# Optimization experiments

Hardware: AMD Instinct MI355X
Metric: run time of the kernel (lower is better)

The kernel has to match this reference:

```python
import jax, jax.numpy as jnp
from jax import lax
import numpy as np

NUM_HEADS = 8
KW = 3  # window kernel size

def _avgpool3(x):
    # x: [B,C,H,W]; AvgPool2d(3,1,1) with count_include_pad=True -> sum/9
    s = lax.reduce_window(x, 0.0, lax.add, (1, 1, KW, KW), (1, 1, 1, 1),
                          ((0, 0), (0, 0), (1, 1), (1, 1)))
    return s / (KW * KW)

def _unfold3(y):
    # y: [B,h,w,C] -> [B,h,w,9,C]; patch index ordered row-major (kh,kw)
    B, h, w, C = y.shape
    yp = jnp.pad(y, ((0, 0), (1, 1), (1, 1), (0, 0)))
    return jnp.stack([yp[:, i:i + h, j:j + w, :]
                      for i in range(KW) for j in range(KW)], axis=3)

def setup_inputs():
    key = jax.random.key(0)
    ks = jax.random.split(key, 9)
    B, C, H, W = 8, 256, 64, 64
    sd = 0.02
    return {
        "x": jax.random.normal(ks[0], (B, C, H, W), jnp.float32),
        "W_qkv": jax.random.normal(ks[1], (4 * C, C), jnp.float32) * sd,
        "b_qkv": jnp.zeros((4 * C,), jnp.float32),
        "W1": jax.random.normal(ks[2], (C // 2, C), jnp.float32) * sd,
        "b1": jnp.zeros((C // 2,), jnp.float32),
        "W2": jax.random.normal(ks[3], (C, C // 2), jnp.float32) * sd,
        "b2": jnp.zeros((C,), jnp.float32),
        "Wp": jax.random.normal(ks[4], (C, C), jnp.float32) * sd,
        "bp": jnp.zeros((C,), jnp.float32),
    }

def reference(x, W_qkv, b_qkv, W1, b1, W2, b2, Wp, bp):
    B, C, H, W = x.shape
    nH = NUM_HEADS
    hd = C // nH
    scale = hd ** -0.5
    # avg pool (stride 1 keeps spatial dims), to channels-last
    y = _avgpool3(x).transpose(0, 2, 3, 1)                 # [B,h,w,C]
    qkv = y @ W_qkv.T + b_qkv                              # [B,h,w,4C]
    qkv = qkv.reshape(B, H, W, C, 4)
    q, k, v, chans = qkv[..., 0], qkv[..., 1], qkv[..., 2], qkv[..., 3]
    # channel gate
    g = jax.nn.sigmoid(jax.nn.relu(chans @ W1.T + b1) @ W2.T + b2)  # [B,h,w,C]
    # local window attention: each query attends to its 3x3 neighborhood
    qh = q.reshape(B, H, W, nH, hd)                        # [B,h,w,n,d]
    kp = _unfold3(k).reshape(B, H, W, KW * KW, nH, hd)     # [B,h,w,9,n,d]
    vp = _unfold3(v).reshape(B, H, W, KW * KW, nH, hd)
    attn = jnp.einsum('bhwnd,bhwknd->bhwnk', qh, kp) * scale
    attn = jax.nn.softmax(attn, axis=-1)
    out = jnp.einsum('bhwnk,bhwknd->bhwnd', attn, vp).reshape(B, H, W, C)
    out = out * g + out
    out = out @ Wp.T + bp
    return out.transpose(0, 3, 1, 2)                       # [B,C,H,W]
```

## Files before the change

### kernel.cpp

```cpp
#include <hip/hip_runtime.h>
#include <stdint.h>

typedef __bf16    bf16x8 __attribute__((ext_vector_type(8)));
typedef float     f32x4  __attribute__((ext_vector_type(4)));
typedef uint32_t  u32x4  __attribute__((ext_vector_type(4)));

#define MFMA(a,b,c) __builtin_amdgcn_mfma_f32_16x16x32_bf16((a),(b),(c),0,0,0)

__device__ __align__(16) uint16_t g_y [8*64*64*256];
__device__ __align__(16) uint16_t g_wpk[393216];

#define WQF 0
#define WKF 65536
#define WVF 131072
#define WCF 196608
#define W1F 262144
#define W2F 294912
#define WPF 327680

static __device__ __forceinline__ float b2f(uint32_t u){ return __builtin_bit_cast(float, u<<16); }
static __device__ __forceinline__ uint32_t f2b(float f){
  uint32_t x = __builtin_bit_cast(uint32_t, f);
  return (x + 0x7fffu + ((x>>16)&1u)) >> 16;
}

__global__ __launch_bounds__(256) void kpack(const float* __restrict__ Wqkv,
    const float* __restrict__ W1, const float* __restrict__ W2,
    const float* __restrict__ Wp){
  int idx = blockIdx.x*256 + threadIdx.x;
  int j = idx & 7, lane = (idx>>3)&63;
  int n16 = lane & 15, q4 = lane>>4;
  float v;
  if (idx < 262144){
    int t = idx >> 16, l = idx & 65535;
    int s = (l>>9)&7, nt = l>>12;
    v = Wqkv[(4*(nt*16+n16) + t)*256 + s*32 + q4*8 + j];
  } else if (idx < 294912){
    int l = idx - 262144;
    int s = (l>>9)&7, nt = l>>12;
    v = W1[(nt*16+n16)*256 + s*32 + q4*8 + j];
  } else if (idx < 327680){
    int l = idx - 294912;
    int s = (l>>9)&3, nt = l>>11;
    v = W2[(nt*16+n16)*128 + s*32 + q4*8 + j];
  } else {
    int l = idx - 327680;
    int s = (l>>9)&7, nt = l>>12;
    v = Wp[(nt*16+n16)*256 + s*32 + q4*8 + j];
  }
  g_wpk[idx] = (uint16_t)f2b(v);
}

__global__ __launch_bounds__(512) void kpool(const float* __restrict__ x){
  __shared__ __align__(16) uint16_t sm[3*256*82];
  uint32_t* smw = (uint32_t*)sm;
  int t = threadIdx.x;
  int b = blockIdx.x >> 6, h = blockIdx.x & 63;
  for (int i=t; i<768; i+=512){
    int base = i*41;
    smw[base+3]  = 0;
    smw[base+36] = 0;
  }
  if (h==0 || h==63){
    int hh = (h==0) ? 0 : 2;
    for (int i=t; i<10496; i+=512) smw[hh*10496 + i] = 0;
  }
  #pragma unroll
  for (int i=0;i<24;i++){
    int id = t + 512*i;
    int w4 = id&15, c = (id>>4)&255, hh = id>>12;
    int gy = h - 1 + hh;
    if ((unsigned)gy < 64u){
      f32x4 ld = *(const f32x4*)&x[(((b*256+c)*64+gy)*64) + w4*4];
      int wb = (((hh*256+c)*82 + 8 + w4*4) >> 1);
      smw[wb+0] = f2b(ld[0]) | (f2b(ld[1])<<16);
      smw[wb+1] = f2b(ld[2]) | (f2b(ld[3])<<16);
    }
  }
  __syncthreads();
  int c = t & 255, wsel = t >> 8;
  int r0 = c*82, r1 = r0 + 256*82, r2 = r1 + 256*82;
  int w0 = wsel*32;
  float csp = b2f(sm[r0+w0+7]) + b2f(sm[r1+w0+7]) + b2f(sm[r2+w0+7]);
  float csc = b2f(sm[r0+w0+8]) + b2f(sm[r1+w0+8]) + b2f(sm[r2+w0+8]);
  uint16_t* dst = g_y + ((b*64+h)*64)*256 + c;
  for (int j2=0;j2<32;j2++){
    int w = w0 + j2;
    float csn = b2f(sm[r0+w+9]) + b2f(sm[r1+w+9]) + b2f(sm[r2+w+9]);
    float yv = (csp + csc + csn) * (1.0f/9.0f);
    dst[w*256] = (uint16_t)f2b(yv);
    csp = csc; csc = csn;
  }
}

#define YSTR 264
#define HSTR 134
#define K2_QS 26400
#define K2_KS 34976
#define K2_VS 48376
#define MCH 0
#define MHS 16896
#define MAO 25600
__global__ __launch_bounds__(512,2) void kattn(const float* __restrict__ bqkv,
    const float* __restrict__ b1, const float* __restrict__ b2v,
    const float* __restrict__ bp, float* __restrict__ out){
  __shared__ __align__(16) uint16_t sm[61776];
  int t = threadIdx.x;
  int lane = t & 63, wave = t >> 6;
  int n16 = lane & 15, quad = lane >> 4;
  int bid = blockIdx.x;
  int bb = bid>>6, tyhi=(bid>>4)&3, txl=(bid>>3)&1, tylo=(bid>>2)&1, txp=bid&3;
  int ty = tyhi*2+tylo, tx = txp*2+txl;

  uint32_t opk[2][16];
  uint32_t chp[32];

  #pragma unroll
  for (int i=0;i<7;i++){
    int id = t + 512*i;
    if (id < 3200){
      int hp = id >> 5, c8 = id & 31;
      int py = hp/10, px = hp - py*10;
      int gy = ty*8 + py - 1, gx = tx*8 + px - 1;
      u32x4 ld = {0,0,0,0};
      if ((unsigned)gy<64u && (unsigned)gx<64u)
        ld = *(const u32x4*)&g_y[((bb*64+gy)*64+gx)*256 + c8*8];
      *(u32x4*)&sm[hp*YSTR + c8*8] = ld;
    }
  }
  __syncthreads();

  #pragma unroll
  for (int hf=0; hf<2; hf++){
    {
      int ntg = hf*8 + wave;
      bf16x8 Bq[8];
      #pragma unroll
      for (int s=0;s<8;s++) Bq[s] = *(const bf16x8*)&g_wpk[WQF + ((ntg*8+s)*64+lane)*8];
      float bq = bqkv[4*(ntg*16+n16) + 0];
      int colB = wave*16;
      #pragma unroll
      for (int mt=0; mt<4; mt++){
        f32x4 a = {0.f,0.f,0.f,0.f};
        int m = mt*16 + n16;
        int hrow = 10*(m>>3) + (m&7) + 11;
        #pragma unroll
        for (int s=0;s<8;s++){
          bf16x8 A = *(const bf16x8*)&sm[hrow*YSTR + s*32 + quad*8];
          a = MFMA(A, Bq[s], a);
        }
        #pragma unroll
        for (int r=0;r<4;r++){
          int row = mt*16 + quad*4 + r;
          sm[K2_QS + row*HSTR + colB + n16] = (uint16_t)f2b(a[r] + bq);
        }
      }
    }
    __syncthreads();
    {
      int ntg = hf*8 + wave;
      bf16x8 Bk[8], Bv[8];
      #pragma unroll
      for (int s=0;s<8;s++){
        Bk[s] = *(const bf16x8*)&g_wpk[WKF + ((ntg*8+s)*64+lane)*8];
        Bv[s] = *(const bf16x8*)&g_wpk[WVF + ((ntg*8+s)*64+lane)*8];
      }
      float bk = bqkv[4*(ntg*16+n16) + 1];
      float bv = bqkv[4*(ntg*16+n16) + 2];
      int colB = wave*16;
      #pragma unroll
      for (int mt=0; mt<7; mt++){
        f32x4 ak = {0.f,0.f,0.f,0.f}, av = {0.f,0.f,0.f,0.f};
        int m = mt*16 + n16;
        int mr = (m < 100) ? m : 99;
        #pragma unroll
        for (int s=0;s<8;s++){
          bf16x8 A = *(const bf16x8*)&sm[mr*YSTR + s*32 + quad*8];
          ak = MFMA(A, Bk[s], ak);
          av = MFMA(A, Bv[s], av);
        }
        #pragma unroll
        for (int r=0;r<4;r++){
          int row = mt*16 + quad*4 + r;
          if (row < 100){
            int py = row/10, px = row - py*10;
            int gy = ty*8 + py - 1, gx = tx*8 + px - 1;
            bool ok = ((unsigned)gy<64u) && ((unsigned)gx<64u);
            float vk = ok ? ak[r] + bk : 0.f;
            float vv = ok ? av[r] + bv : 0.f;
            sm[K2_KS + row*HSTR + colB + n16] = (uint16_t)f2b(vk);
            sm[K2_VS + row*HSTR + colB + n16] = (uint16_t)f2b(vv);
          }
        }
      }
    }
    __syncthreads();
    if (wave < 4){
      int p = t & 63, hl = wave;
      int iy = p >> 3, ix = p & 7;
      int cb = hl*32;
      const uint32_t* q32 = (const uint32_t*)&sm[K2_QS + p*HSTR + cb];
      float qv[32];
      #pragma unroll
      for (int i=0;i<16;i++){ uint32_t u=q32[i]; qv[2*i]=b2f(u&0xffffu); qv[2*i+1]=b2f(u>>16); }
      int hb = (iy+1)*10 + ix + 1;
      const int off[9] = {-11,-10,-9,-1,0,1,9,10,11};
      float sc[9];
      #pragma unroll
      for (int nb=0;nb<9;nb++){
        const uint32_t* k32 = (const uint32_t*)&sm[K2_KS + (hb+off[nb])*HSTR + cb];
        float s = 0.f;
        #pragma unroll
        for (int i=0;i<16;i++){ uint32_t u=k32[i]; s += qv[2*i]*b2f(u&0xffffu) + qv[2*i+1]*b2f(u>>16); }
        sc[nb] = s * 0.17677669529663687f;
      }
      float mx = sc[0];
      #pragma unroll
      for (int nb=1;nb<9;nb++) mx = fmaxf(mx, sc[nb]);
      float l = 0.f;
      #pragma unroll
      for (int nb=0;nb<9;nb++){ sc[nb] = __expf(sc[nb]-mx); l += sc[nb]; }
      float inv = 1.f / l;
      float o[32];
      #pragma unroll
      for (int i=0;i<32;i++) o[i]=0.f;
      #pragma unroll
      for (int nb=0;nb<9;nb++){
        float wgt = sc[nb]*inv;
        const uint32_t* v32 = (const uint32_t*)&sm[K2_VS + (hb+off[nb])*HSTR + cb];
        #pragma unroll
        for (int i=0;i<16;i++){ uint32_t u=v32[i]; o[2*i] += wgt*b2f(u&0xffffu); o[2*i+1] += wgt*b2f(u>>16); }
      }
      #pragma unroll
      for (int i=0;i<16;i++) opk[hf][i] = f2b(o[2*i]) | (f2b(o[2*i+1])<<16);
    } else if (hf == 0){
      #pragma unroll
      for (int jj=0;jj<4;jj++){
        int ntg = (wave-4)*4 + jj;
        bf16x8 Bc[8];
        #pragma unroll
        for (int s=0;s<8;s++) Bc[s] = *(const bf16x8*)&g_wpk[WCF + ((ntg*8+s)*64+lane)*8];
        float bc = bqkv[4*(ntg*16+n16) + 3];
        #pragma unroll
        for (int mt=0; mt<4; mt++){
          f32x4 a = {0.f,0.f,0.f,0.f};
          int m = mt*16 + n16;
          int hrow = 10*(m>>3) + (m&7) + 11;
          #pragma unroll
          for (int s=0;s<8;s++){
            bf16x8 A = *(const bf16x8*)&sm[hrow*YSTR + s*32 + quad*8];
            a = MFMA(A, Bc[s], a);
          }
          chp[(jj*4+mt)*2+0] = f2b(a[0]+bc) | (f2b(a[1]+bc)<<16);
          chp[(jj*4+mt)*2+1] = f2b(a[2]+bc) | (f2b(a[3]+bc)<<16);
        }
      }
    } else {
      #pragma unroll
      for (int jj=0;jj<4;jj++){
        int ntg = (wave-4)*4 + jj;
        int col = ntg*16 + n16;
        #pragma unroll
        for (int mt=0;mt<4;mt++){
          #pragma unroll
          for (int r2=0;r2<2;r2++){
            uint32_t v = chp[(jj*4+mt)*2+r2];
            int row = mt*16 + quad*4 + r2*2;
            sm[MCH + row*264 + col]     = (uint16_t)(v & 0xffffu);
            sm[MCH + (row+1)*264 + col] = (uint16_t)(v >> 16);
          }
        }
      }
    }
    __syncthreads();
  }
  if (wave < 4){
    int p = t & 63, cb = wave*32;
    #pragma unroll
    for (int hf=0;hf<2;hf++)
      #pragma unroll
      for (int i=0;i<16;i++)
        *(uint32_t*)&sm[MAO + p*264 + hf*128 + cb + 2*i] = opk[hf][i];
  }
  {
    int ntg = wave;
    bf16x8 Bf[8];
    #pragma unroll
    for (int s=0;s<8;s++) Bf[s] = *(const bf16x8*)&g_wpk[W1F + ((ntg*8+s)*64+lane)*8];
    float bs = b1[ntg*16+n16];
    int colB = wave*16;
    #pragma unroll
    for (int mt=0;mt<4;mt++){
      f32x4 a = {0.f,0.f,0.f,0.f};
      #pragma unroll
      for (int s=0;s<8;s++){
        bf16x8 A = *(const bf16x8*)&sm[MCH + (mt*16+n16)*264 + s*32 + quad*8];
        a = MFMA(A, Bf[s], a);
      }
      #pragma unroll
      for (int r=0;r<4;r++){
        int row = mt*16 + quad*4 + r;
        sm[MHS + row*136 + colB + n16] = (uint16_t)f2b(fmaxf(a[r]+bs, 0.f));
      }
    }
  }
  __syncthreads();
  #pragma unroll
  for (int jj=0;jj<2;jj++){
    int ntg = wave*2 + jj;
    bf16x8 Bf[4];
    #pragma unroll
    for (int s=0;s<4;s++) Bf[s] = *(const bf16x8*)&g_wpk[W2F + ((ntg*4+s)*64+lane)*8];
    float bs = b2v[ntg*16+n16];
    int colB = ntg*16;
    #pragma unroll
    for (int mt=0;mt<4;mt++){
      f32x4 a = {0.f,0.f,0.f,0.f};
      #pragma unroll
      for (int s=0;s<4;s++){
        bf16x8 A = *(const bf16x8*)&sm[MHS + (mt*16+n16)*136 + s*32 + quad*8];
        a = MFMA(A, Bf[s], a);
      }
      #pragma unroll
      for (int r=0;r<4;r++){
        int row = mt*16 + quad*4 + r;
        float gg = 1.f/(1.f+__expf(-(a[r] + bs)));
        float ao = b2f((uint32_t)sm[MAO + row*264 + colB + n16]);
        sm[MCH + row*264 + colB + n16] = (uint16_t)f2b(ao*(1.f+gg));
      }
    }
  }
  __syncthreads();
  #pragma unroll
  for (int jj=0;jj<2;jj++){
    int ntg = wave*2 + jj;
    bf16x8 Bf[8];
    #pragma unroll
    for (int s=0;s<8;s++) Bf[s] = *(const bf16x8*)&g_wpk[WPF + ((ntg*8+s)*64+lane)*8];
    float bs = bp[ntg*16+n16];
    int colB = ntg*16;
    #pragma unroll
    for (int mt=0;mt<4;mt++){
      f32x4 a = {0.f,0.f,0.f,0.f};
      #pragma unroll
      for (int s=0;s<8;s++){
        bf16x8 A = *(const bf16x8*)&sm[MCH + (mt*16+n16)*264 + s*32 + quad*8];
        a = MFMA(A, Bf[s], a);
      }
      #pragma unroll
      for (int r=0;r<4;r++){
        int row = mt*16 + quad*4 + r;
        sm[MAO + row*264 + colB + n16] = (uint16_t)f2b(a[r]+bs);
      }
    }
  }
  __syncthreads();
  #pragma unroll
  for (int i=0;i<8;i++){
    int idx = t + 512*i;
    int ix4 = idx&1, iy = (idx>>1)&7, c = idx>>4;
    f32x4 stv;
    #pragma unroll
    for (int j=0;j<4;j++){
      int p = iy*8 + ix4*4 + j;
      stv[j] = b2f((uint32_t)sm[MAO + p*264 + c]);
    }
    *(f32x4*)&out[(((bb*256+c)*64) + ty*8+iy)*64 + tx*8 + ix4*4] = stv;
  }
}

extern "C" void kernel_launch(void* const* d_in, const int* in_sizes, int n_in,
                              void* d_out, int out_size, void* d_ws, size_t ws_size,
                              hipStream_t stream){
  (void)in_sizes; (void)n_in; (void)d_ws; (void)ws_size; (void)out_size;
  const float* x    = (const float*)d_in[0];
  const float* Wqkv = (const float*)d_in[1];
  const float* bqkv = (const float*)d_in[2];
  const float* W1   = (const float*)d_in[3];
  const float* b1   = (const float*)d_in[4];
  const float* W2   = (const float*)d_in[5];
  const float* b2   = (const float*)d_in[6];
  const float* Wp   = (const float*)d_in[7];
  const float* bp   = (const float*)d_in[8];
  kpack<<<dim3(1536), dim3(256), 0, stream>>>(Wqkv, W1, W2, Wp);
  kpool<<<dim3(512),  dim3(512), 0, stream>>>(x);
  kattn<<<dim3(512),  dim3(512), 0, stream>>>(bqkv, b1, b2, bp, (float*)d_out);
}
```

Before: 188.4 us.

## Double attention block to 1024 threads and redistribute QKV, attention and gate work

New measurement: 203.5 us. 8.0% more time.

```diff
diff --git a/kernel.cpp b/kernel.cpp
--- a/kernel.cpp
+++ b/kernel.cpp
@@ -19,6 +19,7 @@
 #define WPF 327680
 
 static __device__ __forceinline__ float b2f(uint32_t u){ return __builtin_bit_cast(float, u<<16); }
+static __device__ __forceinline__ float b2fh(uint32_t u){ return __builtin_bit_cast(float, u & 0xffff0000u); }
 static __device__ __forceinline__ uint32_t f2b(float f){
   uint32_t x = __builtin_bit_cast(uint32_t, f);
   return (x + 0x7fffu + ((x>>16)&1u)) >> 16;
@@ -94,17 +95,18 @@
 }
 
 #define YSTR 264
-#define HSTR 134
-#define K2_QS 26400
-#define K2_KS 34976
-#define K2_VS 48376
+#define HSTR 136
+#define YS 0
+#define QS 26400
+#define KS 35104
+#define VS 48704
 #define MCH 0
 #define MHS 16896
-#define MAO 25600
-__global__ __launch_bounds__(512,2) void kattn(const float* __restrict__ bqkv,
+#define MAO 26400
+__global__ __launch_bounds__(1024,4) void kattn(const float* __restrict__ bqkv,
     const float* __restrict__ b1, const float* __restrict__ b2v,
     const float* __restrict__ bp, float* __restrict__ out){
-  __shared__ __align__(16) uint16_t sm[61776];
+  __shared__ __align__(16) uint16_t sm[62304];
   int t = threadIdx.x;
   int lane = t & 63, wave = t >> 6;
   int n16 = lane & 15, quad = lane >> 4;
@@ -112,12 +114,12 @@
   int bb = bid>>6, tyhi=(bid>>4)&3, txl=(bid>>3)&1, tylo=(bid>>2)&1, txp=bid&3;
   int ty = tyhi*2+tylo, tx = txp*2+txl;
 
-  uint32_t opk[2][16];
-  uint32_t chp[32];
+  uint32_t opk[2][8];
+  uint32_t chp[16];
 
   #pragma unroll
-  for (int i=0;i<7;i++){
-    int id = t + 512*i;
+  for (int i=0;i<4;i++){
+    int id = t + 1024*i;
     if (id < 3200){
       int hp = id >> 5, c8 = id & 31;
       int py = hp/10, px = hp - py*10;
@@ -133,87 +135,97 @@
   #pragma unroll
   for (int hf=0; hf<2; hf++){
     {
-      int ntg = hf*8 + wave;
-      bf16x8 Bq[8];
-      #pragma unroll
-      for (int s=0;s<8;s++) Bq[s] = *(const bf16x8*)&g_wpk[WQF + ((ntg*8+s)*64+lane)*8];
-      float bq = bqkv[4*(ntg*16+n16) + 0];
-      int colB = wave*16;
-      #pragma unroll
-      for (int mt=0; mt<4; mt++){
-        f32x4 a = {0.f,0.f,0.f,0.f};
-        int m = mt*16 + n16;
-        int hrow = 10*(m>>3) + (m&7) + 11;
-        #pragma unroll
-        for (int s=0;s<8;s++){
-          bf16x8 A = *(const bf16x8*)&sm[hrow*YSTR + s*32 + quad*8];
-          a = MFMA(A, Bq[s], a);
-        }
-        #pragma unroll
-        for (int r=0;r<4;r++){
-          int row = mt*16 + quad*4 + r;
-          sm[K2_QS + row*HSTR + colB + n16] = (uint16_t)f2b(a[r] + bq);
+      int ntg = wave & 7;
+      int ntgg = hf*8 + ntg;
+      bool isK = wave < 8;
+      int colB = ntg*16;
+      {
+        bf16x8 Bx[8];
+        const uint16_t* wb = &g_wpk[(isK?WKF:WVF)];
+        #pragma unroll
+        for (int s=0;s<8;s++) Bx[s] = *(const bf16x8*)&wb[((ntgg*8+s)*64+lane)*8];
+        float bx = bqkv[4*(ntgg*16+n16) + (isK?1:2)];
+        int base = isK ? KS : VS;
+        #pragma unroll
+        for (int mt=0; mt<7; mt++){
+          f32x4 a = {0.f,0.f,0.f,0.f};
+          int m = mt*16 + n16;
+          int mr = (m < 100) ? m : 99;
+          #pragma unroll
+          for (int s=0;s<8;s++){
+            bf16x8 A = *(const bf16x8*)&sm[YS + mr*YSTR + s*32 + quad*8];
+            a = MFMA(A, Bx[s], a);
+          }
+          #pragma unroll
+          for (int r=0;r<4;r++){
+            int row = mt*16 + quad*4 + r;
+            if (row < 100){
+              int py = row/10, px = row - py*10;
+              int gy = ty*8 + py - 1, gx = tx*8 + px - 1;
+              bool ok = ((unsigned)gy<64u) && ((unsigned)gx<64u);
+              sm[base + row*HSTR + colB + n16] = (uint16_t)f2b(ok ? a[r]+bx : 0.f);
+            }
+          }
+        }
+      }
+      {
+        bf16x8 Bq[8];
+        #pragma unroll
+        for (int s=0;s<8;s++) Bq[s] = *(const bf16x8*)&g_wpk[WQF + ((ntgg*8+s)*64+lane)*8];
+        float bq = bqkv[4*(ntgg*16+n16) + 0];
+        int mt0 = isK ? 0 : 2;
+        #pragma unroll
+        for (int mi=0; mi<2; mi++){
+          int mt = mt0 + mi;
+          f32x4 a = {0.f,0.f,0.f,0.f};
+          int m = mt*16 + n16;
+          int hrow = 10*(m>>3) + (m&7) + 11;
+          #pragma unroll
+          for (int s=0;s<8;s++){
+            bf16x8 A = *(const bf16x8*)&sm[YS + hrow*YSTR + s*32 + quad*8];
+            a = MFMA(A, Bq[s], a);
+          }
+          #pragma unroll
+          for (int r=0;r<4;r++){
+            int row = mt*16 + quad*4 + r;
+            sm[QS + row*HSTR + colB + n16] = (uint16_t)f2b(a[r] + bq);
+          }
         }
       }
     }
     __syncthreads();
-    {
-      int ntg = hf*8 + wave;
-      bf16x8 Bk[8], Bv[8];
-      #pragma unroll
-      for (int s=0;s<8;s++){
-        Bk[s] = *(const bf16x8*)&g_wpk[WKF + ((ntg*8+s)*64+lane)*8];
-        Bv[s] = *(const bf16x8*)&g_wpk[WVF + ((ntg*8+s)*64+lane)*8];
-      }
-      float bk = bqkv[4*(ntg*16+n16) + 1];
-      float bv = bqkv[4*(ntg*16+n16) + 2];
-      int colB = wave*16;
-      #pragma unroll
-      for (int mt=0; mt<7; mt++){
-        f32x4 ak = {0.f,0.f,0.f,0.f}, av = {0.f,0.f,0.f,0.f};
-        int m = mt*16 + n16;
-        int mr = (m < 100) ? m : 99;
-        #pragma unroll
-        for (int s=0;s<8;s++){
-          bf16x8 A = *(const bf16x8*)&sm[mr*YSTR + s*32 + quad*8];
-          ak = MFMA(A, Bk[s], ak);
-          av = MFMA(A, Bv[s], av);
-        }
-        #pragma unroll
-        for (int r=0;r<4;r++){
-          int row = mt*16 + quad*4 + r;
-          if (row < 100){
-            int py = row/10, px = row - py*10;
-            int gy = ty*8 + py - 1, gx = tx*8 + px - 1;
-            bool ok = ((unsigned)gy<64u) && ((unsigned)gx<64u);
-            float vk = ok ? ak[r] + bk : 0.f;
-            float vv = ok ? av[r] + bv : 0.f;
-            sm[K2_KS + row*HSTR + colB + n16] = (uint16_t)f2b(vk);
-            sm[K2_VS + row*HSTR + colB + n16] = (uint16_t)f2b(vv);
-          }
-        }
-      }
-    }
-    __syncthreads();
-    if (wave < 4){
-      int p = t & 63, hl = wave;
+    if (wave < 8){
+      int h = wave >> 1, ph = wave & 1;
+      int pl = lane & 31, dh = lane >> 5;
+      int p = ph*32 + pl;
       int iy = p >> 3, ix = p & 7;
-      int cb = hl*32;
-      const uint32_t* q32 = (const uint32_t*)&sm[K2_QS + p*HSTR + cb];
-      float qv[32];
-      #pragma unroll
-      for (int i=0;i<16;i++){ uint32_t u=q32[i]; qv[2*i]=b2f(u&0xffffu); qv[2*i+1]=b2f(u>>16); }
+      int co = h*32 + dh*16;
+      u32x4 qa = *(const u32x4*)&sm[QS + p*HSTR + co];
+      u32x4 qb = *(const u32x4*)&sm[QS + p*HSTR + co + 8];
+      float qv[16];
+      #pragma unroll
+      for (int i=0;i<4;i++){
+        qv[2*i]   = b2f(qa[i]);  qv[2*i+1]   = b2fh(qa[i]);
+        qv[8+2*i] = b2f(qb[i]);  qv[8+2*i+1] = b2fh(qb[i]);
+      }
       int hb = (iy+1)*10 + ix + 1;
       const int off[9] = {-11,-10,-9,-1,0,1,9,10,11};
       float sc[9];
       #pragma unroll
       for (int nb=0;nb<9;nb++){
-        const uint32_t* k32 = (const uint32_t*)&sm[K2_KS + (hb+off[nb])*HSTR + cb];
+        const uint16_t* kr = &sm[KS + (hb+off[nb])*HSTR + co];
+        u32x4 ka = *(const u32x4*)kr;
+        u32x4 kb = *(const u32x4*)(kr+8);
         float s = 0.f;
         #pragma unroll
-        for (int i=0;i<16;i++){ uint32_t u=k32[i]; s += qv[2*i]*b2f(u&0xffffu) + qv[2*i+1]*b2f(u>>16); }
-        sc[nb] = s * 0.17677669529663687f;
-      }
+        for (int i=0;i<4;i++){
+          s += qv[2*i]*b2f(ka[i]) + qv[2*i+1]*b2fh(ka[i]);
+          s += qv[8+2*i]*b2f(kb[i]) + qv[8+2*i+1]*b2fh(kb[i]);
+        }
+        sc[nb] = s;
+      }
+      #pragma unroll
+      for (int nb=0;nb<9;nb++) sc[nb] = (sc[nb] + __shfl_xor(sc[nb], 32)) * 0.17677669529663687f;
       float mx = sc[0];
       #pragma unroll
       for (int nb=1;nb<9;nb++) mx = fmaxf(mx, sc[nb]);
@@ -221,22 +233,27 @@
       #pragma unroll
       for (int nb=0;nb<9;nb++){ sc[nb] = __expf(sc[nb]-mx); l += sc[nb]; }
       float inv = 1.f / l;
-      float o[32];
-      #pragma unroll
-      for (int i=0;i<32;i++) o[i]=0.f;
+      float o[16];
+      #pragma unroll
+      for (int i=0;i<16;i++) o[i]=0.f;
       #pragma unroll
       for (int nb=0;nb<9;nb++){
         float wgt = sc[nb]*inv;
-        const uint32_t* v32 = (const uint32_t*)&sm[K2_VS + (hb+off[nb])*HSTR + cb];
-        #pragma unroll
-        for (int i=0;i<16;i++){ uint32_t u=v32[i]; o[2*i] += wgt*b2f(u&0xffffu); o[2*i+1] += wgt*b2f(u>>16); }
-      }
-      #pragma unroll
-      for (int i=0;i<16;i++) opk[hf][i] = f2b(o[2*i]) | (f2b(o[2*i+1])<<16);
+        const uint16_t* vr = &sm[VS + (hb+off[nb])*HSTR + co];
+        u32x4 va = *(const u32x4*)vr;
+        u32x4 vb = *(const u32x4*)(vr+8);
+        #pragma unroll
+        for (int i=0;i<4;i++){
+          o[2*i]     += wgt*b2f(va[i]);  o[2*i+1]   += wgt*b2fh(va[i]);
+          o[8+2*i]   += wgt*b2f(vb[i]);  o[8+2*i+1] += wgt*b2fh(vb[i]);
+        }
+      }
+      #pragma unroll
+      for (int i=0;i<8;i++) opk[hf][i] = f2b(o[2*i]) | (f2b(o[2*i+1])<<16);
     } else if (hf == 0){
       #pragma unroll
-      for (int jj=0;jj<4;jj++){
-        int ntg = (wave-4)*4 + jj;
+      for (int jj=0;jj<2;jj++){
+        int ntg = (wave-8)*2 + jj;
         bf16x8 Bc[8];
         #pragma unroll
         for (int s=0;s<8;s++) Bc[s] = *(const bf16x8*)&g_wpk[WCF + ((ntg*8+s)*64+lane)*8];
@@ -248,7 +265,7 @@
           int hrow = 10*(m>>3) + (m&7) + 11;
           #pragma unroll
           for (int s=0;s<8;s++){
-            bf16x8 A = *(const bf16x8*)&sm[hrow*YSTR + s*32 + quad*8];
+            bf16x8 A = *(const bf16x8*)&sm[YS + hrow*YSTR + s*32 + quad*8];
             a = MFMA(A, Bc[s], a);
           }
           chp[(jj*4+mt)*2+0] = f2b(a[0]+bc) | (f2b(a[1]+bc)<<16);
@@ -257,8 +274,8 @@
       }
     } else {
       #pragma unroll
-      for (int jj=0;jj<4;jj++){
-        int ntg = (wave-4)*4 + jj;
+      for (int jj=0;jj<2;jj++){
+        int ntg = (wave-8)*2 + jj;
         int col = ntg*16 + n16;
         #pragma unroll
         for (int mt=0;mt<4;mt++){
@@ -266,76 +283,78 @@
           for (int r2=0;r2<2;r2++){
             uint32_t v = chp[(jj*4+mt)*2+r2];
             int row = mt*16 + quad*4 + r2*2;
-            sm[MCH + row*264 + col]     = (uint16_t)(v & 0xffffu);
-            sm[MCH + (row+1)*264 + col] = (uint16_t)(v >> 16);
+            sm[MCH + row*YSTR + col]        = (uint16_t)(v & 0xffffu);
+            sm[MCH + (row+1)*YSTR + col]    = (uint16_t)(v >> 16);
           }
         }
       }
     }
     __syncthreads();
   }
-  if (wave < 4){
-    int p = t & 63, cb = wave*32;
-    #pragma unroll
-    for (int hf=0;hf<2;hf++)
-      #pragma unroll
-      for (int i=0;i<16;i++)
-        *(uint32_t*)&sm[MAO + p*264 + hf*128 + cb + 2*i] = opk[hf][i];
-  }
+  if (wave < 8){
+    int h = wave >> 1, ph = wave & 1;
+    int pl = lane & 31, dh = lane >> 5;
+    int p = ph*32 + pl;
+    int co = h*32 + dh*16;
+    #pragma unroll
+    for (int hf=0;hf<2;hf++){
+      u32x4 s0 = {opk[hf][0],opk[hf][1],opk[hf][2],opk[hf][3]};
+      u32x4 s1 = {opk[hf][4],opk[hf][5],opk[hf][6],opk[hf][7]};
+      *(u32x4*)&sm[MAO + p*YSTR + hf*128 + co]     = s0;
+      *(u32x4*)&sm[MAO + p*YSTR + hf*128 + co + 8] = s1;
+    }
+  } else {
+    int ntg = wave - 8;
+    bf16x8 Bf[8];
+    #pragma unroll
+    for (int s=0;s<8;s++) Bf[s] = *(const bf16x8*)&g_wpk[W1F + ((ntg*8+s)*64+lane)*8];
+    float bs = b1[ntg*16+n16];
+    int colB = ntg*16;
+    #pragma unroll
+    for (int mt=0;mt<4;mt++){
+      f32x4 a = {0.f,0.f,0.f,0.f};
+      #pragma unroll
+      for (int s=0;s<8;s++){
+        bf16x8 A = *(const bf16x8*)&sm[MCH + (mt*16+n16)*YSTR + s*32 + quad*8];
+        a = MFMA(A, Bf[s], a);
+      }
+      #pragma unroll
+      for (int r=0;r<4;r++){
+        int row = mt*16 + quad*4 + r;
+        sm[MHS + row*HSTR + colB + n16] = (uint16_t)f2b(fmaxf(a[r]+bs, 0.f));
+      }
+    }
+  }
+  __syncthreads();
+  {
+    int ntg = wave;
+    bf16x8 Bf[4];
+    #pragma unroll
+    for (int s=0;s<4;s++) Bf[s] = *(const bf16x8*)&g_wpk[W2F + ((ntg*4+s)*64+lane)*8];
+    float bs = b2v[ntg*16+n16];
+    int colB = ntg*16;
+    #pragma unroll
+    for (int mt=0;mt<4;mt++){
+      f32x4 a = {0.f,0.f,0.f,0.f};
+      #pragma unroll
+      for (int s=0;s<4;s++){
+        bf16x8 A = *(const bf16x8*)&sm[MHS + (mt*16+n16)*HSTR + s*32 + quad*8];
+        a = MFMA(A, Bf[s], a);
+      }
+      #pragma unroll
+      for (int r=0;r<4;r++){
+        int row = mt*16 + quad*4 + r;
+        float gg = 1.f/(1.f+__expf(-(a[r] + bs)));
+        float ao = b2f((uint32_t)sm[MAO + row*YSTR + colB + n16]);
+        sm[MCH + row*YSTR + colB + n16] = (uint16_t)f2b(ao*(1.f+gg));
+      }
+    }
+  }
+  __syncthreads();
   {
     int ntg = wave;
     bf16x8 Bf[8];
     #pragma unroll
-    for (int s=0;s<8;s++) Bf[s] = *(const bf16x8*)&g_wpk[W1F + ((ntg*8+s)*64+lane)*8];
-    float bs = b1[ntg*16+n16];
-    int colB = wave*16;
-    #pragma unroll
-    for (int mt=0;mt<4;mt++){
-      f32x4 a = {0.f,0.f,0.f,0.f};
-      #pragma unroll
-      for (int s=0;s<8;s++){
-        bf16x8 A = *(const bf16x8*)&sm[MCH + (mt*16+n16)*264 + s*32 + quad*8];
-        a = MFMA(A, Bf[s], a);
-      }
-      #pragma unroll
-      for (int r=0;r<4;r++){
-        int row = mt*16 + quad*4 + r;
-        sm[MHS + row*136 + colB + n16] = (uint16_t)f2b(fmaxf(a[r]+bs, 0.f));
-      }
-    }
-  }
-  __syncthreads();
-  #pragma unroll
-  for (int jj=0;jj<2;jj++){
-    int ntg = wave*2 + jj;
-    bf16x8 Bf[4];
-    #pragma unroll
-    for (int s=0;s<4;s++) Bf[s] = *(const bf16x8*)&g_wpk[W2F + ((ntg*4+s)*64+lane)*8];
-    float bs = b2v[ntg*16+n16];
-    int colB = ntg*16;
-    #pragma unroll
-    for (int mt=0;mt<4;mt++){
-      f32x4 a = {0.f,0.f,0.f,0.f};
-      #pragma unroll
-      for (int s=0;s<4;s++){
-        bf16x8 A = *(const bf16x8*)&sm[MHS + (mt*16+n16)*136 + s*32 + quad*8];
-        a = MFMA(A, Bf[s], a);
-      }
-      #pragma unroll
-      for (int r=0;r<4;r++){
-        int row = mt*16 + quad*4 + r;
-        float gg = 1.f/(1.f+__expf(-(a[r] + bs)));
-        float ao = b2f((uint32_t)sm[MAO + row*264 + colB + n16]);
-        sm[MCH + row*264 + colB + n16] = (uint16_t)f2b(ao*(1.f+gg));
-      }
-    }
-  }
-  __syncthreads();
-  #pragma unroll
-  for (int jj=0;jj<2;jj++){
-    int ntg = wave*2 + jj;
-    bf16x8 Bf[8];
-    #pragma unroll
     for (int s=0;s<8;s++) Bf[s] = *(const bf16x8*)&g_wpk[WPF + ((ntg*8+s)*64+lane)*8];
     float bs = bp[ntg*16+n16];
     int colB = ntg*16;
@@ -344,26 +363,26 @@
       f32x4 a = {0.f,0.f,0.f,0.f};
       #pragma unroll
       for (int s=0;s<8;s++){
-        bf16x8 A = *(const bf16x8*)&sm[MCH + (mt*16+n16)*264 + s*32 + quad*8];
+        bf16x8 A = *(const bf16x8*)&sm[MCH + (mt*16+n16)*YSTR + s*32 + quad*8];
         a = MFMA(A, Bf[s], a);
       }
       #pragma unroll
       for (int r=0;r<4;r++){
         int row = mt*16 + quad*4 + r;
-        sm[MAO + row*264 + colB + n16] = (uint16_t)f2b(a[r]+bs);
+        sm[MAO + row*YSTR + colB + n16] = (uint16_t)f2b(a[r]+bs);
       }
     }
   }
   __syncthreads();
   #pragma unroll
-  for (int i=0;i<8;i++){
-    int idx = t + 512*i;
+  for (int i=0;i<4;i++){
+    int idx = t + 1024*i;
     int ix4 = idx&1, iy = (idx>>1)&7, c = idx>>4;
     f32x4 stv;
     #pragma unroll
     for (int j=0;j<4;j++){
       int p = iy*8 + ix4*4 + j;
-      stv[j] = b2f((uint32_t)sm[MAO + p*264 + c]);
+      stv[j] = b2f((uint32_t)sm[MAO + p*YSTR + c]);
     }
     *(f32x4*)&out[(((bb*256+c)*64) + ty*8+iy)*64 + tx*8 + ix4*4] = stv;
   }
@@ -384,5 +403,5 @@
   const float* bp   = (const float*)d_in[8];
   kpack<<<dim3(1536), dim3(256), 0, stream>>>(Wqkv, W1, W2, Wp);
   kpool<<<dim3(512),  dim3(512), 0, stream>>>(x);
-  kattn<<<dim3(512),  dim3(512), 0, stream>>>(bqkv, b1, b2, bp, (float*)d_out);
+  kattn<<<dim3(512),  dim3(1024), 0, stream>>>(bqkv, b1, b2, bp, (float*)d_out);
 }
```
